# Kernel tuning notes

Measured on AMD Instinct MI355X. Metric: run time of the kernel, lower is better.

Reference implementation:

```python
import jax, jax.numpy as jnp
import numpy as np

B, T_IN, T_OUT, F, H = 256, 336, 96, 32, 256


def _lstm_cell(x_t, h, c, Wih, Whh, b):
    # PyTorch gate order: input, forget, cell(g), output
    gates = x_t @ Wih.T + h @ Whh.T + b  # [B, 4H]
    i, f, g, o = jnp.split(gates, 4, axis=-1)
    c_new = jax.nn.sigmoid(f) * c + jax.nn.sigmoid(i) * jnp.tanh(g)
    h_new = jax.nn.sigmoid(o) * jnp.tanh(c_new)
    return h_new, c_new


def setup_inputs() -> dict:
    key = jax.random.key(0)
    ks = jax.random.split(key, 16)
    s = 0.05  # keep recurrence numerically tame
    g = lambda k, shape: (jax.random.normal(k, shape) * s).astype(jnp.float32)
    return {
        "x": jax.random.normal(ks[0], (B, T_IN, F), dtype=jnp.float32),
        "enc_Wih0": g(ks[1], (4 * H, F)),
        "enc_Whh0": g(ks[2], (4 * H, H)),
        "enc_b0": g(ks[3], (4 * H,)),
        "enc_Wih1": g(ks[4], (4 * H, H)),
        "enc_Whh1": g(ks[5], (4 * H, H)),
        "enc_b1": g(ks[6], (4 * H,)),
        "dec_Wih0": g(ks[7], (4 * H, F)),
        "dec_Whh0": g(ks[8], (4 * H, H)),
        "dec_b0": g(ks[9], (4 * H,)),
        "dec_Wih1": g(ks[10], (4 * H, H)),
        "dec_Whh1": g(ks[11], (4 * H, H)),
        "dec_b1": g(ks[12], (4 * H,)),
        "dec_Wout": g(ks[13], (F, H)),
        "dec_bout": g(ks[14], (F,)),
    }


def reference(x, enc_Wih0, enc_Whh0, enc_b0, enc_Wih1, enc_Whh1, enc_b1,
              dec_Wih0, dec_Whh0, dec_b0, dec_Wih1, dec_Whh1, dec_b1,
              dec_Wout, dec_bout):
    batch = x.shape[0]
    zeros = jnp.zeros((batch, H), dtype=x.dtype)

    # --- encoder: step-by-step 2-layer LSTM over input sequence ---
    def enc_step(carry, x_t):
        h0, c0, h1, c1 = carry
        h0, c0 = _lstm_cell(x_t, h0, c0, enc_Wih0, enc_Whh0, enc_b0)
        h1, c1 = _lstm_cell(h0, h1, c1, enc_Wih1, enc_Whh1, enc_b1)
        return (h0, c0, h1, c1), None

    xs = jnp.swapaxes(x, 0, 1)  # [T_IN, B, F]
    (h0, c0, h1, c1), _ = jax.lax.scan(enc_step, (zeros, zeros, zeros, zeros), xs)

    def dec_step(carry, _):
        h0, c0, h1, c1, y = carry
        h0, c0 = _lstm_cell(y, h0, c0, dec_Wih0, dec_Whh0, dec_b0)
        h1, c1 = _lstm_cell(h0, h1, c1, dec_Wih1, dec_Whh1, dec_b1)
        y = h1 @ dec_Wout.T + dec_bout  # project hidden -> feature dim
        return (h0, c0, h1, c1, y), y

    y0 = x[:, -1, :]  # [B, F]
    _, ys = jax.lax.scan(dec_step, (h0, c0, h1, c1, y0), None, length=T_OUT)
    return jnp.swapaxes(ys, 0, 1)  # [B, T_OUT, F]
```

## Files before the change

kernel.cpp:

```cpp
#include <hip/hip_runtime.h>
#include <hip/hip_bf16.h>

#define BB   256
#define TIN  336
#define TOUT 96
#define FF   32
#define HH   256

#define NGS 16
#define NBG 16
#define RPG 16
#define TPB 512

#define KB0 9
#define KB1 16
#define ASTRIDE 520
#define XSTRIDE 40

#define N_L0  (16*4*KB0*64*8)
#define N_L1  (16*4*KB1*64*8)
#define U_E0  0
#define U_E1  (U_E0 + N_L0)
#define U_D0  (U_E1 + N_L1)
#define U_D1  (U_D0 + N_L1)
#define U_END (U_D1 + N_L1)
#define HPAR  65536
#define U_H0  U_END
#define U_H1  (U_H0 + 2*HPAR)
#define U_HD  (U_H1 + 2*HPAR)
#define U_CTR (U_HD + 2*HPAR)
#define U_ZEND (U_CTR + 16384)

#define GATE(bias, g, r, cc) (bias[(g)*16 + (cc)] + pbuf[0][r][(g)*16 + (cc)] + pbuf[1][r][(g)*16 + (cc)])

typedef __bf16 bf16x8 __attribute__((ext_vector_type(8)));
typedef float  f32x4  __attribute__((ext_vector_type(4)));

__device__ __forceinline__ float sigf(float x) { return 1.f / (1.f + __expf(-x)); }
__device__ __forceinline__ float tanhfast(float x) { return 1.f - 2.f / (__expf(2.f * x) + 1.f); }
__device__ __forceinline__ unsigned short f2bf(float f) {
    union { float f; unsigned u; } v; v.f = f;
    unsigned r = v.u + 0x7FFF + ((v.u >> 16) & 1);
    return (unsigned short)(r >> 16);
}
__device__ __forceinline__ uint4 ldg_sc(const void* p) {
    uint4 v;
    asm volatile("global_load_dwordx4 %0, %1, off sc0 sc1\n\ts_waitcnt vmcnt(0)"
                 : "=v"(v) : "v"(p) : "memory");
    return v;
}
__device__ __forceinline__ void ldg_sc2(const void* p0, const void* p1, uint4& a, uint4& b) {
    asm volatile("global_load_dwordx4 %0, %2, off sc0 sc1\n\t"
                 "global_load_dwordx4 %1, %3, off sc0 sc1\n\t"
                 "s_waitcnt vmcnt(0)"
                 : "=v"(a), "=v"(b) : "v"(p0), "v"(p1) : "memory");
}

__global__ void prep_kernel(const float* __restrict__ eWih0, const float* __restrict__ eWhh0,
                            const float* __restrict__ eWih1, const float* __restrict__ eWhh1,
                            const float* __restrict__ dWih0, const float* __restrict__ dWhh0,
                            const float* __restrict__ dWih1, const float* __restrict__ dWhh1,
                            const float* __restrict__ Wout,  float* __restrict__ wsf)
{
    unsigned short* wsu = (unsigned short*)wsf;
    for (long u = (long)blockIdx.x * blockDim.x + threadIdx.x; u < (long)U_END;
         u += (long)gridDim.x * blockDim.x) {
        int region; long l;
        if (u < U_E1)      { region = 0; l = u - U_E0; }
        else if (u < U_D0) { region = 1; l = u - U_E1; }
        else if (u < U_D1) { region = 2; l = u - U_D0; }
        else               { region = 3; l = u - U_D1; }
        const int KB = (region == 0) ? KB0 : KB1;
        int j = (int)(l & 7), lane = (int)((l >> 3) & 63);
        long rem = l >> 9;
        int kb = (int)(rem % KB), q = (int)(rem / KB);
        int nt = q & 3, gi = q >> 2;
        int k  = kb * 32 + ((lane >> 4) << 3) + j;
        int gj = nt * 256 + gi * 16 + (lane & 15);
        float v;
        if (region == 0)      v = (k < 32)  ? eWih0[gj * 32 + k]  : eWhh0[gj * 256 + (k - 32)];
        else if (region == 1) v = (k < 256) ? eWih1[gj * 256 + k] : eWhh1[gj * 256 + (k - 256)];
        else if (region == 2) {
            if (k < 256) v = dWhh0[gj * 256 + k];
            else {
                float acc = 0.f; int kk = k - 256;
                #pragma unroll 8
                for (int f = 0; f < 32; ++f) acc += dWih0[gj * 32 + f] * Wout[f * 256 + kk];
                v = acc;
            }
        } else                v = (k < 256) ? dWih1[gj * 256 + k] : dWhh1[gj * 256 + (k - 256)];
        wsu[u] = f2bf(v);
    }
    for (long z = (long)blockIdx.x * blockDim.x + threadIdx.x; z < (long)(4 * HPAR);
         z += (long)gridDim.x * blockDim.x)
        wsu[U_H0 + z] = 0;
    for (long z = (long)blockIdx.x * blockDim.x + threadIdx.x; z < 16384;
         z += (long)gridDim.x * blockDim.x)
        wsu[U_CTR + z] = 0;
}

__global__ __launch_bounds__(TPB) void lstm_main(
    const float* __restrict__ x,
    const float* __restrict__ eb0, const float* __restrict__ eb1,
    const float* __restrict__ db0, const float* __restrict__ db1,
    const float* __restrict__ Wout, const float* __restrict__ bout,
    const float* __restrict__ dWih0,
    float* __restrict__ ws, float* __restrict__ out)
{
    const int gi = blockIdx.x >> 4;
    const int gb = blockIdx.x & 15;

    unsigned short* wsu = (unsigned short*)ws;
    const unsigned short* h0u = wsu + U_H0;
    const unsigned short* h1u = wsu + U_H1;
    const unsigned short* hdu = wsu + U_HD;
    unsigned* h0d = (unsigned*)(wsu + U_H0);
    unsigned* h1d = (unsigned*)(wsu + U_H1);
    unsigned* hdd = (unsigned*)(wsu + U_HD);
    unsigned* flg = (unsigned*)(wsu + U_CTR) + gb * 512;

    const int t  = threadIdx.x;
    const int wv = t >> 6;
    const int ln = t & 63;
    const int nt = wv & 3, w2 = wv >> 2;
    const int arow = ln & 15, ak = (ln >> 4) << 3;

    __shared__ __align__(16) unsigned short Atile[16 * ASTRIDE];
    __shared__ __align__(16) unsigned short Xtile[16 * XSTRIDE];
    __shared__ float pbuf[2][16][68];
    __shared__ float cst[2][16][16];
    __shared__ float sb[5][64];

    if (t < 64) {
        int gj = (t >> 4) * 256 + gi * 16 + (t & 15);
        sb[0][t] = eb0[gj]; sb[1][t] = eb1[gj]; sb[3][t] = db1[gj]; sb[4][t] = db0[gj];
        float be = db0[gj];
        #pragma unroll 8
        for (int f = 0; f < 32; ++f) be += dWih0[gj * 32 + f] * bout[f];
        sb[2][t] = be;
    }
    if (t < 256) { cst[0][t >> 4][t & 15] = 0.f; cst[1][t >> 4][t & 15] = 0.f; }

    bf16x8 B0[8], B1[8];
    const int kbs0 = w2 ? 4 : 0, kbn0 = w2 ? 5 : 4;
    const int kbs1 = w2 ? 8 : 0;
    auto loadB = [&](size_t ubase, int KB, int kbs, int kbn, bf16x8* Breg) {
        #pragma unroll
        for (int i = 0; i < 8; ++i)
            if (i < kbn)
                Breg[i] = *(const bf16x8*)(wsu + ubase +
                            ((size_t)(nt * KB + kbs + i) * 64 + ln) * 8);
    };

    int posts = 0;
    auto gsync = [&]() {
        ++posts;
        if (t == 0)
            __hip_atomic_store(flg + gi * 32, (unsigned)posts, __ATOMIC_RELAXED,
                               __HIP_MEMORY_SCOPE_AGENT);
        if (wv == 0) {
            for (;;) {
                unsigned v = __hip_atomic_load(flg + (ln & 15) * 32, __ATOMIC_RELAXED,
                                               __HIP_MEMORY_SCOPE_AGENT);
                if (__all((int)(v >= (unsigned)posts))) break;
                __builtin_amdgcn_s_sleep(1);
            }
        }
        __syncthreads();
    };

    auto phase = [&](const bf16x8* Breg, int kbs, int kbn, bool withX, const float* bias,
                     int layer, unsigned* hdstDw, bool addY0, bool drain) {
        f32x4 acc = {0.f, 0.f, 0.f, 0.f};
        #pragma unroll
        for (int i = 0; i < 8; ++i) {
            if (i < kbn) {
                const int kb = kbs + i;
                bf16x8 a;
                if (withX && kb == 0) a = *(const bf16x8*)(Xtile + arow * XSTRIDE + ak);
                else {
                    const int koff = (withX ? (kb - 1) : kb) * 32;
                    a = *(const bf16x8*)(Atile + arow * ASTRIDE + koff + ak);
                }
                acc = __builtin_amdgcn_mfma_f32_16x16x32_bf16(a, Breg[i], acc, 0, 0, 0);
            }
        }
        #pragma unroll
        for (int rg = 0; rg < 4; ++rg)
            pbuf[w2][(ln >> 4) * 4 + rg][nt * 16 + arow] = acc[rg];
        __syncthreads();
        if (t < 128) {
            const int r = t >> 3, c2 = t & 7;
            const int c0 = c2 * 2, c1 = c0 + 1;
            float xi0 = GATE(bias, 0, r, c0), xf0 = GATE(bias, 1, r, c0);
            float xg0 = GATE(bias, 2, r, c0), xo0 = GATE(bias, 3, r, c0);
            float xi1 = GATE(bias, 0, r, c1), xf1 = GATE(bias, 1, r, c1);
            float xg1 = GATE(bias, 2, r, c1), xo1 = GATE(bias, 3, r, c1);
            if (addY0) {
                const float* xp = x + ((size_t)(gb * RPG + r) * TIN + (TIN - 1)) * FF;
                float xr[32];
                #pragma unroll
                for (int f = 0; f < 32; ++f) xr[f] = xp[f];
                #pragma unroll
                for (int g = 0; g < 4; ++g) {
                    const float* w0 = dWih0 + (size_t)(g * 256 + gi * 16 + c0) * 32;
                    const float* w1 = dWih0 + (size_t)(g * 256 + gi * 16 + c1) * 32;
                    float a0 = 0.f, a1 = 0.f;
                    #pragma unroll
                    for (int f = 0; f < 32; ++f) {
                        a0 = fmaf(w0[f], xr[f], a0);
                        a1 = fmaf(w1[f], xr[f], a1);
                    }
                    if (g == 0) { xi0 += a0; xi1 += a1; }
                    else if (g == 1) { xf0 += a0; xf1 += a1; }
                    else if (g == 2) { xg0 += a0; xg1 += a1; }
                    else { xo0 += a0; xo1 += a1; }
                }
            }
            float ca = cst[layer][r][c0], cb = cst[layer][r][c1];
            float cn0 = sigf(xf0) * ca + sigf(xi0) * tanhfast(xg0);
            float cn1 = sigf(xf1) * cb + sigf(xi1) * tanhfast(xg1);
            cst[layer][r][c0] = cn0; cst[layer][r][c1] = cn1;
            float h0v = sigf(xo0) * tanhfast(cn0);
            float h1v = sigf(xo1) * tanhfast(cn1);
            unsigned pv = (unsigned)f2bf(h0v) | ((unsigned)f2bf(h1v) << 16);
            __hip_atomic_store(hdstDw + (size_t)(gb * RPG + r) * 128 + gi * 8 + c2, pv,
                               __ATOMIC_RELAXED, __HIP_MEMORY_SCOPE_AGENT);
        }
        if (drain) asm volatile("s_waitcnt vmcnt(0)" : : : "memory");
        __syncthreads();
    };

    loadB(U_E0 + (size_t)gi * 18432, KB0, kbs0, kbn0, B0);
    loadB(U_E1 + (size_t)gi * 32768, KB1, kbs1, 8,    B1);
    { const int r = t >> 5, c8 = t & 31;
      uint4 z = {0u, 0u, 0u, 0u};
      *(uint4*)(Atile + r * ASTRIDE + c8 * 8) = z;
      Xtile[r * XSTRIDE + c8] = f2bf(x[((size_t)(gb * RPG + r) * TIN) * FF + c8]); }
    __syncthreads();

    for (int s = 0; s < TIN; ++s) {
        const int rp = s & 1, wp = rp ^ 1;
        phase(B0, kbs0, kbn0, true, sb[0], 0, h0d + (size_t)wp * (HPAR / 2), false, true);
        {
            const int r = t >> 5, c8 = t & 31;
            const int xs = (s + 1 < TIN) ? s + 1 : -1;
            float xv = 0.f;
            if (xs >= 0) xv = x[((size_t)(gb * RPG + r) * TIN + xs) * FF + c8];
            gsync();
            uint4 a, b;
            ldg_sc2(h0u + (size_t)wp * HPAR + (size_t)(gb * RPG + r) * 256 + c8 * 8,
                    h1u + (size_t)rp * HPAR + (size_t)(gb * RPG + r) * 256 + c8 * 8, a, b);
            *(uint4*)(Atile + r * ASTRIDE + c8 * 8) = a;
            *(uint4*)(Atile + r * ASTRIDE + 256 + c8 * 8) = b;
            if (xs >= 0) Xtile[r * XSTRIDE + c8] = f2bf(xv);
            __syncthreads();
        }
        phase(B1, kbs1, 8, false, sb[1], 1, h1d + (size_t)wp * (HPAR / 2),
              false, s == TIN - 1);
    }

    loadB(U_D0 + (size_t)gi * 32768, KB1, kbs1, 8, B0);
    loadB(U_D1 + (size_t)gi * 32768, KB1, kbs1, 8, B1);
    const int yr = t >> 5, yfq = (t >> 4) & 1, ykc = t & 15;
    const int yf = gi * 2 + yfq;
    float wreg[16];
    #pragma unroll
    for (int i = 0; i < 16; ++i) wreg[i] = Wout[(size_t)yf * 256 + ykc * 16 + i];
    const float ybo = bout[yf];
    auto ycompute = [&](int td) {
        const unsigned* ap = (const unsigned*)(Atile + yr * ASTRIDE + 256 + ykc * 16);
        float a = 0.f;
        #pragma unroll
        for (int j = 0; j < 8; ++j) {
            unsigned w = ap[j];
            a = fmaf(__uint_as_float(w << 16),         wreg[2 * j],     a);
            a = fmaf(__uint_as_float(w & 0xffff0000u), wreg[2 * j + 1], a);
        }
        #pragma unroll
        for (int off = 1; off < 16; off <<= 1) a += __shfl_xor(a, off, 64);
        if (ykc == 0)
            out[((size_t)(gb * RPG + yr) * TOUT + td) * FF + yf] = a + ybo;
    };

    for (int td = 0; td < TOUT; ++td) {
        const int s = TIN + td;
        const int wp = (s & 1) ^ 1;
        gsync();
        {
            const int r = t >> 5, c8 = t & 31;
            if (td == 0) {
                uint4 z = {0u, 0u, 0u, 0u};
                *(uint4*)(Atile + r * ASTRIDE + 256 + c8 * 8) = z;
            } else {
                uint4 a = ldg_sc(hdu + (size_t)((td - 1) & 1) * HPAR +
                                 (size_t)(gb * RPG + r) * 256 + c8 * 8);
                *(uint4*)(Atile + r * ASTRIDE + 256 + c8 * 8) = a;
            }
            __syncthreads();
        }
        if (td > 0) ycompute(td - 1);
        phase(B0, kbs1, 8, false, (td == 0) ? sb[4] : sb[2], 0,
              h0d + (size_t)wp * (HPAR / 2), td == 0, true);
        gsync();
        {
            const int r = t >> 5, c8 = t & 31;
            if (td == 0) {
                uint4 a, b;
                ldg_sc2(h0u + (size_t)wp * HPAR + (size_t)(gb * RPG + r) * 256 + c8 * 8,
                        h1u + 0 * HPAR  + (size_t)(gb * RPG + r) * 256 + c8 * 8,
                        a, b);
                *(uint4*)(Atile + r * ASTRIDE + c8 * 8) = a;
                *(uint4*)(Atile + r * ASTRIDE + 256 + c8 * 8) = b;
            } else {
                uint4 a = ldg_sc(h0u + (size_t)wp * HPAR +
                                 (size_t)(gb * RPG + r) * 256 + c8 * 8);
                *(uint4*)(Atile + r * ASTRIDE + c8 * 8) = a;
            }
            __syncthreads();
        }
        phase(B1, kbs1, 8, false, sb[3], 1, hdd + (size_t)(td & 1) * (HPAR / 2),
              false, true);
    }

    gsync();
    {
        const int r = t >> 5, c8 = t & 31;
        uint4 a = ldg_sc(hdu + (size_t)((TOUT - 1) & 1) * HPAR +
                         (size_t)(gb * RPG + r) * 256 + c8 * 8);
        *(uint4*)(Atile + r * ASTRIDE + 256 + c8 * 8) = a;
        __syncthreads();
    }
    ycompute(TOUT - 1);
}

extern "C" void kernel_launch(void* const* d_in, const int* in_sizes, int n_in,
                              void* d_out, int out_size, void* d_ws, size_t ws_size,
                              hipStream_t stream) {
    const float* x     = (const float*)d_in[0];
    const float* eWih0 = (const float*)d_in[1];
    const float* eWhh0 = (const float*)d_in[2];
    const float* eb0   = (const float*)d_in[3];
    const float* eWih1 = (const float*)d_in[4];
    const float* eWhh1 = (const float*)d_in[5];
    const float* eb1   = (const float*)d_in[6];
    const float* dWih0 = (const float*)d_in[7];
    const float* dWhh0 = (const float*)d_in[8];
    const float* db0   = (const float*)d_in[9];
    const float* dWih1 = (const float*)d_in[10];
    const float* dWhh1 = (const float*)d_in[11];
    const float* db1   = (const float*)d_in[12];
    const float* dWout = (const float*)d_in[13];
    const float* dbout = (const float*)d_in[14];
    float* ws = (float*)d_ws;
    float* out = (float*)d_out;

    prep_kernel<<<1024, 256, 0, stream>>>(eWih0, eWhh0, eWih1, eWhh1,
                                          dWih0, dWhh0, dWih1, dWhh1, dWout, ws);
    lstm_main<<<NGS * NBG, TPB, 0, stream>>>(x, eb0, eb1, db0, db1,
                                             dWout, dbout, dWih0, ws, out);
}
```

Measured before the change: 1.737 ms.

## Wavefront-pipeline encoder layers so one grid sync covers both layers per step

```diff
diff --git a/kernel.cpp b/kernel.cpp
--- a/kernel.cpp
+++ b/kernel.cpp
@@ -14,8 +14,8 @@
 
 #define KB0 9
 #define KB1 16
-#define ASTRIDE 520
-#define XSTRIDE 40
+#define AST 260
+#define XST 40
 
 #define N_L0  (16*4*KB0*64*8)
 #define N_L1  (16*4*KB1*64*8)
@@ -29,9 +29,9 @@
 #define U_H1  (U_H0 + 2*HPAR)
 #define U_HD  (U_H1 + 2*HPAR)
 #define U_CTR (U_HD + 2*HPAR)
-#define U_ZEND (U_CTR + 16384)
-
-#define GATE(bias, g, r, cc) (bias[(g)*16 + (cc)] + pbuf[0][r][(g)*16 + (cc)] + pbuf[1][r][(g)*16 + (cc)])
+#define U_ZEND (U_CTR + 4096)
+
+#define GATE(L, bias, g, r, cc) (bias[(g)*16 + (cc)] + pbuf[L][0][r][(g)*16 + (cc)] + pbuf[L][1][r][(g)*16 + (cc)])
 
 typedef __bf16 bf16x8 __attribute__((ext_vector_type(8)));
 typedef float  f32x4  __attribute__((ext_vector_type(4)));
@@ -94,7 +94,7 @@
     for (long z = (long)blockIdx.x * blockDim.x + threadIdx.x; z < (long)(4 * HPAR);
          z += (long)gridDim.x * blockDim.x)
         wsu[U_H0 + z] = 0;
-    for (long z = (long)blockIdx.x * blockDim.x + threadIdx.x; z < 16384;
+    for (long z = (long)blockIdx.x * blockDim.x + threadIdx.x; z < 4096;
          z += (long)gridDim.x * blockDim.x)
         wsu[U_CTR + z] = 0;
 }
@@ -117,7 +117,9 @@
     unsigned* h0d = (unsigned*)(wsu + U_H0);
     unsigned* h1d = (unsigned*)(wsu + U_H1);
     unsigned* hdd = (unsigned*)(wsu + U_HD);
-    unsigned* flg = (unsigned*)(wsu + U_CTR) + gb * 512;
+    unsigned* flgA = (unsigned*)(wsu + U_CTR) + gb * 96;
+    unsigned* flgB = flgA + 32;
+    unsigned* flgD = flgA + 64;
 
     const int t  = threadIdx.x;
     const int wv = t >> 6;
@@ -125,9 +127,10 @@
     const int nt = wv & 3, w2 = wv >> 2;
     const int arow = ln & 15, ak = (ln >> 4) << 3;
 
-    __shared__ __align__(16) unsigned short Atile[16 * ASTRIDE];
-    __shared__ __align__(16) unsigned short Xtile[16 * XSTRIDE];
-    __shared__ float pbuf[2][16][68];
+    __shared__ __align__(16) unsigned short AH0[16 * AST];
+    __shared__ __align__(16) unsigned short AH1[16 * AST];
+    __shared__ __align__(16) unsigned short Xt[16 * XST];
+    __shared__ float pbuf[2][2][16][68];
     __shared__ float cst[2][16][16];
     __shared__ float sb[5][64];
 
@@ -152,50 +155,175 @@
                             ((size_t)(nt * KB + kbs + i) * 64 + ln) * 8);
     };
 
-    int posts = 0;
-    auto gsync = [&]() {
-        ++posts;
+    auto mfmaB0 = [&]() {
+        f32x4 acc = {0.f, 0.f, 0.f, 0.f};
+        #pragma unroll
+        for (int i = 0; i < 8; ++i) {
+            if (i < kbn0) {
+                const int kb = kbs0 + i;
+                bf16x8 a;
+                if (kb == 0) a = *(const bf16x8*)(Xt + arow * XST + ak);
+                else         a = *(const bf16x8*)(AH0 + arow * AST + (kb - 1) * 32 + ak);
+                acc = __builtin_amdgcn_mfma_f32_16x16x32_bf16(a, B0[i], acc, 0, 0, 0);
+            }
+        }
+        #pragma unroll
+        for (int rg = 0; rg < 4; ++rg)
+            pbuf[0][w2][(ln >> 4) * 4 + rg][nt * 16 + arow] = acc[rg];
+    };
+    auto mfmaK512 = [&](const bf16x8* Breg, int ph) {
+        f32x4 acc = {0.f, 0.f, 0.f, 0.f};
+        #pragma unroll
+        for (int i = 0; i < 8; ++i) {
+            const int kb = kbs1 + i;
+            bf16x8 a;
+            if (kb < 8) a = *(const bf16x8*)(AH0 + arow * AST + kb * 32 + ak);
+            else        a = *(const bf16x8*)(AH1 + arow * AST + (kb - 8) * 32 + ak);
+            acc = __builtin_amdgcn_mfma_f32_16x16x32_bf16(a, Breg[i], acc, 0, 0, 0);
+        }
+        #pragma unroll
+        for (int rg = 0; rg < 4; ++rg)
+            pbuf[ph][w2][(ln >> 4) * 4 + rg][nt * 16 + arow] = acc[rg];
+    };
+
+    auto cellSlot = [&](int L, int q, const float* bias, unsigned* dstDw) {
+        const int r = q >> 3, c2 = q & 7;
+        const int c0 = c2 * 2, c1 = c0 + 1;
+        float xi0 = GATE(L, bias, 0, r, c0), xf0 = GATE(L, bias, 1, r, c0);
+        float xg0 = GATE(L, bias, 2, r, c0), xo0 = GATE(L, bias, 3, r, c0);
+        float xi1 = GATE(L, bias, 0, r, c1), xf1 = GATE(L, bias, 1, r, c1);
+        float xg1 = GATE(L, bias, 2, r, c1), xo1 = GATE(L, bias, 3, r, c1);
+        float ca = cst[L][r][c0], cb = cst[L][r][c1];
+        float cn0 = sigf(xf0) * ca + sigf(xi0) * tanhfast(xg0);
+        float cn1 = sigf(xf1) * cb + sigf(xi1) * tanhfast(xg1);
+        cst[L][r][c0] = cn0; cst[L][r][c1] = cn1;
+        float h0v = sigf(xo0) * tanhfast(cn0);
+        float h1v = sigf(xo1) * tanhfast(cn1);
+        unsigned pv = (unsigned)f2bf(h0v) | ((unsigned)f2bf(h1v) << 16);
+        __hip_atomic_store(dstDw + (size_t)(gb * RPG + r) * 128 + gi * 8 + c2, pv,
+                           __ATOMIC_RELAXED, __HIP_MEMORY_SCOPE_AGENT);
+    };
+
+    const unsigned* ppoll;
+    bool pexempt;
+    if (ln < 16)      { ppoll = flgA + ln;        pexempt = (ln == gi); }
+    else if (ln < 32) { ppoll = flgB + (ln - 16); pexempt = ((ln - 16) == gi); }
+    else              { ppoll = flgA + gi;        pexempt = true; }
+
+    loadB(U_E0 + (size_t)gi * 18432, KB0, kbs0, kbn0, B0);
+    loadB(U_E1 + (size_t)gi * 32768, KB1, kbs1, 8,    B1);
+    { const int r = t >> 5, c8 = t & 31;
+      uint4 z = {0u, 0u, 0u, 0u};
+      *(uint4*)(AH0 + r * AST + c8 * 8) = z;
+      Xt[r * XST + c8] = f2bf(x[((size_t)(gb * RPG + r) * TIN) * FF + c8]); }
+    __syncthreads();
+
+    for (int s = 0; s < TIN; ++s) {
+        mfmaB0();
+        if (s > 0) mfmaK512(B1, 1);
+        const int r5 = t >> 5, c85 = t & 31;
+        const int xs = (s + 1 < TIN) ? s + 1 : -1;
+        float xv = 0.f;
+        if (xs >= 0) xv = x[((size_t)(gb * RPG + r5) * TIN + xs) * FF + c85];
+        __syncthreads();
+        if (wv == 0) {
+            cellSlot(0, ln,      sb[0], h0d + (size_t)(s & 1) * (HPAR / 2));
+            cellSlot(0, ln + 64, sb[0], h0d + (size_t)(s & 1) * (HPAR / 2));
+            asm volatile("s_waitcnt vmcnt(0)" ::: "memory");
+            if (ln == 0)
+                __hip_atomic_store(flgA + gi, (unsigned)(s + 1), __ATOMIC_RELAXED,
+                                   __HIP_MEMORY_SCOPE_AGENT);
+        } else if (wv == 1) {
+            if (s > 0) {
+                cellSlot(1, ln,      sb[1], h1d + (size_t)((s - 1) & 1) * (HPAR / 2));
+                cellSlot(1, ln + 64, sb[1], h1d + (size_t)((s - 1) & 1) * (HPAR / 2));
+            }
+            asm volatile("s_waitcnt vmcnt(0)" ::: "memory");
+            if (ln == 0)
+                __hip_atomic_store(flgB + gi, (unsigned)(s + 1), __ATOMIC_RELAXED,
+                                   __HIP_MEMORY_SCOPE_AGENT);
+        } else if (wv == 7) {
+            const unsigned tgt = (unsigned)(s + 1);
+            for (;;) {
+                unsigned v = __hip_atomic_load(ppoll, __ATOMIC_RELAXED,
+                                               __HIP_MEMORY_SCOPE_AGENT);
+                if (__all((int)(pexempt || v >= tgt))) break;
+                __builtin_amdgcn_s_sleep(1);
+            }
+        }
+        __syncthreads();
+        {
+            uint4 a, b;
+            ldg_sc2(h0u + (size_t)(s & 1) * HPAR + (size_t)(gb * RPG + r5) * 256 + c85 * 8,
+                    h1u + (size_t)((s - 1) & 1) * HPAR + (size_t)(gb * RPG + r5) * 256 + c85 * 8,
+                    a, b);
+            *(uint4*)(AH0 + r5 * AST + c85 * 8) = a;
+            *(uint4*)(AH1 + r5 * AST + c85 * 8) = b;
+            if (xs >= 0) Xt[r5 * XST + c85] = f2bf(xv);
+        }
+        __syncthreads();
+    }
+
+    {
+        mfmaK512(B1, 1);
+        __syncthreads();
+        if (t < 128)
+            cellSlot(1, t, sb[1], h1d + (size_t)((TIN - 1) & 1) * (HPAR / 2));
+        asm volatile("s_waitcnt vmcnt(0)" ::: "memory");
+        __syncthreads();
+    }
+
+    loadB(U_D0 + (size_t)gi * 32768, KB1, kbs1, 8, B0);
+    loadB(U_D1 + (size_t)gi * 32768, KB1, kbs1, 8, B1);
+    const int yr = t >> 5, yfq = (t >> 4) & 1, ykc = t & 15;
+    const int yf = gi * 2 + yfq;
+    float wreg[16];
+    #pragma unroll
+    for (int i = 0; i < 16; ++i) wreg[i] = Wout[(size_t)yf * 256 + ykc * 16 + i];
+    const float ybo = bout[yf];
+    auto ycompute = [&](int td) {
+        const unsigned* ap = (const unsigned*)(AH1 + yr * AST + ykc * 16);
+        float a = 0.f;
+        #pragma unroll
+        for (int j = 0; j < 8; ++j) {
+            unsigned w = ap[j];
+            a = fmaf(__uint_as_float(w << 16),         wreg[2 * j],     a);
+            a = fmaf(__uint_as_float(w & 0xffff0000u), wreg[2 * j + 1], a);
+        }
+        #pragma unroll
+        for (int off = 1; off < 16; off <<= 1) a += __shfl_xor(a, off, 64);
+        if (ykc == 0)
+            out[((size_t)(gb * RPG + yr) * TOUT + td) * FF + yf] = a + ybo;
+    };
+
+    int postsD = 0;
+    auto gsyncD = [&]() {
+        ++postsD;
         if (t == 0)
-            __hip_atomic_store(flg + gi * 32, (unsigned)posts, __ATOMIC_RELAXED,
+            __hip_atomic_store(flgD + gi, (unsigned)postsD, __ATOMIC_RELAXED,
                                __HIP_MEMORY_SCOPE_AGENT);
         if (wv == 0) {
             for (;;) {
-                unsigned v = __hip_atomic_load(flg + (ln & 15) * 32, __ATOMIC_RELAXED,
+                unsigned v = __hip_atomic_load(flgD + (ln & 15), __ATOMIC_RELAXED,
                                                __HIP_MEMORY_SCOPE_AGENT);
-                if (__all((int)(v >= (unsigned)posts))) break;
+                if (__all((int)(v >= (unsigned)postsD))) break;
                 __builtin_amdgcn_s_sleep(1);
             }
         }
         __syncthreads();
     };
 
-    auto phase = [&](const bf16x8* Breg, int kbs, int kbn, bool withX, const float* bias,
-                     int layer, unsigned* hdstDw, bool addY0, bool drain) {
-        f32x4 acc = {0.f, 0.f, 0.f, 0.f};
-        #pragma unroll
-        for (int i = 0; i < 8; ++i) {
-            if (i < kbn) {
-                const int kb = kbs + i;
-                bf16x8 a;
-                if (withX && kb == 0) a = *(const bf16x8*)(Xtile + arow * XSTRIDE + ak);
-                else {
-                    const int koff = (withX ? (kb - 1) : kb) * 32;
-                    a = *(const bf16x8*)(Atile + arow * ASTRIDE + koff + ak);
-                }
-                acc = __builtin_amdgcn_mfma_f32_16x16x32_bf16(a, Breg[i], acc, 0, 0, 0);
-            }
-        }
-        #pragma unroll
-        for (int rg = 0; rg < 4; ++rg)
-            pbuf[w2][(ln >> 4) * 4 + rg][nt * 16 + arow] = acc[rg];
+    auto phaseD = [&](const bf16x8* Breg, const float* bias, int layer,
+                      unsigned* hdstDw, bool addY0) {
+        mfmaK512(Breg, 0);
         __syncthreads();
         if (t < 128) {
             const int r = t >> 3, c2 = t & 7;
             const int c0 = c2 * 2, c1 = c0 + 1;
-            float xi0 = GATE(bias, 0, r, c0), xf0 = GATE(bias, 1, r, c0);
-            float xg0 = GATE(bias, 2, r, c0), xo0 = GATE(bias, 3, r, c0);
-            float xi1 = GATE(bias, 0, r, c1), xf1 = GATE(bias, 1, r, c1);
-            float xg1 = GATE(bias, 2, r, c1), xo1 = GATE(bias, 3, r, c1);
+            float xi0 = GATE(0, bias, 0, r, c0), xf0 = GATE(0, bias, 1, r, c0);
+            float xg0 = GATE(0, bias, 2, r, c0), xo0 = GATE(0, bias, 3, r, c0);
+            float xi1 = GATE(0, bias, 0, r, c1), xf1 = GATE(0, bias, 1, r, c1);
+            float xg1 = GATE(0, bias, 2, r, c1), xo1 = GATE(0, bias, 3, r, c1);
             if (addY0) {
                 const float* xp = x + ((size_t)(gb * RPG + r) * TIN + (TIN - 1)) * FF;
                 float xr[32];
@@ -227,108 +355,55 @@
             __hip_atomic_store(hdstDw + (size_t)(gb * RPG + r) * 128 + gi * 8 + c2, pv,
                                __ATOMIC_RELAXED, __HIP_MEMORY_SCOPE_AGENT);
         }
-        if (drain) asm volatile("s_waitcnt vmcnt(0)" : : : "memory");
-        __syncthreads();
-    };
-
-    loadB(U_E0 + (size_t)gi * 18432, KB0, kbs0, kbn0, B0);
-    loadB(U_E1 + (size_t)gi * 32768, KB1, kbs1, 8,    B1);
-    { const int r = t >> 5, c8 = t & 31;
-      uint4 z = {0u, 0u, 0u, 0u};
-      *(uint4*)(Atile + r * ASTRIDE + c8 * 8) = z;
-      Xtile[r * XSTRIDE + c8] = f2bf(x[((size_t)(gb * RPG + r) * TIN) * FF + c8]); }
-    __syncthreads();
-
-    for (int s = 0; s < TIN; ++s) {
-        const int rp = s & 1, wp = rp ^ 1;
-        phase(B0, kbs0, kbn0, true, sb[0], 0, h0d + (size_t)wp * (HPAR / 2), false, true);
-        {
-            const int r = t >> 5, c8 = t & 31;
-            const int xs = (s + 1 < TIN) ? s + 1 : -1;
-            float xv = 0.f;
-            if (xs >= 0) xv = x[((size_t)(gb * RPG + r) * TIN + xs) * FF + c8];
-            gsync();
-            uint4 a, b;
-            ldg_sc2(h0u + (size_t)wp * HPAR + (size_t)(gb * RPG + r) * 256 + c8 * 8,
-                    h1u + (size_t)rp * HPAR + (size_t)(gb * RPG + r) * 256 + c8 * 8, a, b);
-            *(uint4*)(Atile + r * ASTRIDE + c8 * 8) = a;
-            *(uint4*)(Atile + r * ASTRIDE + 256 + c8 * 8) = b;
-            if (xs >= 0) Xtile[r * XSTRIDE + c8] = f2bf(xv);
-            __syncthreads();
-        }
-        phase(B1, kbs1, 8, false, sb[1], 1, h1d + (size_t)wp * (HPAR / 2),
-              false, s == TIN - 1);
-    }
-
-    loadB(U_D0 + (size_t)gi * 32768, KB1, kbs1, 8, B0);
-    loadB(U_D1 + (size_t)gi * 32768, KB1, kbs1, 8, B1);
-    const int yr = t >> 5, yfq = (t >> 4) & 1, ykc = t & 15;
-    const int yf = gi * 2 + yfq;
-    float wreg[16];
-    #pragma unroll
-    for (int i = 0; i < 16; ++i) wreg[i] = Wout[(size_t)yf * 256 + ykc * 16 + i];
-    const float ybo = bout[yf];
-    auto ycompute = [&](int td) {
-        const unsigned* ap = (const unsigned*)(Atile + yr * ASTRIDE + 256 + ykc * 16);
-        float a = 0.f;
-        #pragma unroll
-        for (int j = 0; j < 8; ++j) {
-            unsigned w = ap[j];
-            a = fmaf(__uint_as_float(w << 16),         wreg[2 * j],     a);
-            a = fmaf(__uint_as_float(w & 0xffff0000u), wreg[2 * j + 1], a);
-        }
-        #pragma unroll
-        for (int off = 1; off < 16; off <<= 1) a += __shfl_xor(a, off, 64);
-        if (ykc == 0)
-            out[((size_t)(gb * RPG + yr) * TOUT + td) * FF + yf] = a + ybo;
+        asm volatile("s_waitcnt vmcnt(0)" : : : "memory");
+        __syncthreads();
     };
 
     for (int td = 0; td < TOUT; ++td) {
         const int s = TIN + td;
         const int wp = (s & 1) ^ 1;
-        gsync();
+        gsyncD();
         {
             const int r = t >> 5, c8 = t & 31;
             if (td == 0) {
                 uint4 z = {0u, 0u, 0u, 0u};
-                *(uint4*)(Atile + r * ASTRIDE + 256 + c8 * 8) = z;
+                *(uint4*)(AH1 + r * AST + c8 * 8) = z;
             } else {
                 uint4 a = ldg_sc(hdu + (size_t)((td - 1) & 1) * HPAR +
                                  (size_t)(gb * RPG + r) * 256 + c8 * 8);
-                *(uint4*)(Atile + r * ASTRIDE + 256 + c8 * 8) = a;
+                *(uint4*)(AH1 + r * AST + c8 * 8) = a;
             }
             __syncthreads();
         }
         if (td > 0) ycompute(td - 1);
-        phase(B0, kbs1, 8, false, (td == 0) ? sb[4] : sb[2], 0,
-              h0d + (size_t)wp * (HPAR / 2), td == 0, true);
-        gsync();
+        phaseD(B0, (td == 0) ? sb[4] : sb[2], 0,
+               h0d + (size_t)wp * (HPAR / 2), td == 0);
+        gsyncD();
         {
             const int r = t >> 5, c8 = t & 31;
             if (td == 0) {
                 uint4 a, b;
                 ldg_sc2(h0u + (size_t)wp * HPAR + (size_t)(gb * RPG + r) * 256 + c8 * 8,
-                        h1u + 0 * HPAR  + (size_t)(gb * RPG + r) * 256 + c8 * 8,
-                        a, b);
-                *(uint4*)(Atile + r * ASTRIDE + c8 * 8) = a;
-                *(uint4*)(Atile + r * ASTRIDE + 256 + c8 * 8) = b;
+                        h1u + (size_t)((TIN - 1) & 1) * HPAR  +
+                            (size_t)(gb * RPG + r) * 256 + c8 * 8, a, b);
+                *(uint4*)(AH0 + r * AST + c8 * 8) = a;
+                *(uint4*)(AH1 + r * AST + c8 * 8) = b;
             } else {
                 uint4 a = ldg_sc(h0u + (size_t)wp * HPAR +
                                  (size_t)(gb * RPG + r) * 256 + c8 * 8);
-                *(uint4*)(Atile + r * ASTRIDE + c8 * 8) = a;
+                *(uint4*)(AH0 + r * AST + c8 * 8) = a;
             }
             __syncthreads();
         }
-        phase(B1, kbs1, 8, false, sb[3], 1, hdd + (size_t)(td & 1) * (HPAR / 2),
-              false, true);
-    }
-
-    gsync();
+        phaseD(B1, sb[3], 1, hdd + (size_t)(td & 1) * (HPAR / 2), false);
+    }
+
+    gsyncD();
     {
         const int r = t >> 5, c8 = t & 31;
         uint4 a = ldg_sc(hdu + (size_t)((TOUT - 1) & 1) * HPAR +
                          (size_t)(gb * RPG + r) * 256 + c8 * 8);
-        *(uint4*)(Atile + r * ASTRIDE + 256 + c8 * 8) = a;
+        *(uint4*)(AH1 + r * AST + c8 * 8) = a;
         __syncthreads();
     }
     ycompute(TOUT - 1);
```

Result: no change. 1.766 ms (+1.7%).
